# Performance work log

Measured on AMD Instinct MI355X. Metric: run time of the kernel, lower is better.

Reference implementation:

```python
import jax, jax.numpy as jnp
import numpy as np

L, B, T, D, H, M = 2, 4, 1024, 256, 4, 1024
EPS = 1e-5  # hk.LayerNorm default


def setup_inputs() -> dict:
    key = jax.random.key(0)
    ks = jax.random.split(key, 12)
    s_in = (2.0 / D) ** 0.5       # VarianceScaling(2.0), fan_in = D
    s_o = (2.0 / (H * D)) ** 0.5  # fan_in = H*D for final projection
    s_m = (1.0 / M) ** 0.5
    g = lambda k, shape, s: jax.random.normal(k, shape, jnp.float32) * s
    return {
        "queries": g(ks[0], (B, T, D), 1.0),
        "Wq": g(ks[1], (L, D, H * D), s_in),
        "bq": jnp.zeros((L, H * D), jnp.float32),
        "Wk": g(ks[2], (L, D, H * D), s_in),
        "bk": jnp.zeros((L, H * D), jnp.float32),
        "Wv": g(ks[3], (L, D, H * D), s_in),
        "bv": jnp.zeros((L, H * D), jnp.float32),
        "Wo": g(ks[4], (L, H * D, D), s_o),
        "bo": jnp.zeros((L, D), jnp.float32),
        "ln1_s": jnp.ones((L, D), jnp.float32),
        "ln1_b": jnp.zeros((L, D), jnp.float32),
        "W1": g(ks[5], (L, D, M), s_in),
        "b1": jnp.zeros((L, M), jnp.float32),
        "W2": g(ks[6], (L, M, D), s_m),
        "b2": jnp.zeros((L, D), jnp.float32),
        "ln2_s": jnp.ones((L, D), jnp.float32),
        "ln2_b": jnp.zeros((L, D), jnp.float32),
    }


def _layernorm(x, s, o):
    m = jnp.mean(x, axis=-1, keepdims=True)
    v = jnp.var(x, axis=-1, keepdims=True)
    return (x - m) * jax.lax.rsqrt(v + EPS) * s + o


def _block(x, Wq, bq, Wk, bk, Wv, bv, Wo, bo, ln1_s, ln1_b, W1, b1, W2, b2, ln2_s, ln2_b):
    # Multi-head self-attention with per-head dim = D (key_size == qkv_size)
    q = (x @ Wq + bq).reshape(B, T, H, D)
    k = (x @ Wk + bk).reshape(B, T, H, D)
    v = (x @ Wv + bv).reshape(B, T, H, D)
    q = q / jnp.sqrt(jnp.float32(D))
    attn = jnp.einsum('bqhd,bkhd->bhqk', q, k)   # [B,H,T,T]
    attn = jax.nn.softmax(attn, axis=-1)
    o = jnp.einsum('bhqk,bkhd->bqhd', attn, v).reshape(B, T, H * D)
    o = o @ Wo + bo
    # post-norm residual 1
    x = _layernorm(o + x, ln1_s, ln1_b)
    # MLP: Linear(D->M) + ReLU + Linear(M->D)
    h = jax.nn.relu(x @ W1 + b1)
    m = h @ W2 + b2
    return _layernorm(m + x, ln2_s, ln2_b)


def reference(queries, Wq, bq, Wk, bk, Wv, bv, Wo, bo, ln1_s, ln1_b,
              W1, b1, W2, b2, ln2_s, ln2_b):
    x = queries
    for i in range(L):
        x = _block(x, Wq[i], bq[i], Wk[i], bk[i], Wv[i], bv[i], Wo[i], bo[i],
                   ln1_s[i], ln1_b[i], W1[i], b1[i], W2[i], b2[i],
                   ln2_s[i], ln2_b[i])
    return x
```

## Files before the change

kernel.cpp:

```cpp
#include <hip/hip_runtime.h>
#include <hip/hip_bf16.h>

#define CL 2
#define CB 4
#define CT 1024
#define CD 256
#define CH 4
#define CM 1024
#define CHD (CH * CD)
#define NROW (CB * CT)

typedef unsigned short ushort_t;
typedef __attribute__((ext_vector_type(8))) short short8v;
typedef __attribute__((ext_vector_type(4))) float float4v;

#define LOG2E 1.44269504088896f

__device__ __forceinline__ float bf2f(unsigned short u) {
    return __uint_as_float(((unsigned int)u) << 16);
}
__device__ __forceinline__ unsigned short f2bf(float f) {
    unsigned int x = __float_as_uint(f);
    return (unsigned short)((x + 0x7fffu + ((x >> 16) & 1u)) >> 16);
}

__global__ __launch_bounds__(256) void detect_kernel(
    const ushort_t* __restrict__ w, int n, int* __restrict__ flag)
{
    __shared__ int red[256];
    int c = 0;
    for (int i = threadIdx.x; i < n; i += 256) {
        float v = bf2f(w[i]);
        if (!(fabsf(v) <= 1e6f)) c++;
    }
    red[threadIdx.x] = c;
    __syncthreads();
    for (int s = 128; s > 0; s >>= 1) {
        if (threadIdx.x < s) red[threadIdx.x] += red[threadIdx.x + s];
        __syncthreads();
    }
    if (threadIdx.x == 0) flag[0] = (red[0] < 8) ? 1 : 0;
}

__global__ __launch_bounds__(256) void tconv_all(
    const void* __restrict__ Wq, const void* __restrict__ Wk,
    const void* __restrict__ Wv, const void* __restrict__ W1,
    ushort_t* __restrict__ wqkvT, ushort_t* __restrict__ w1T,
    const int* __restrict__ flagp)
{
    const int fbf = *flagp;
    const int z = blockIdx.z;
    const int which = z >> 1, l = z & 1;
    const void* in = (which == 0) ? Wq : (which == 1) ? Wk
                   : (which == 2) ? Wv : W1;
    ushort_t* out = (which < 3)
        ? wqkvT + (long)l * 3072 * 256 + (long)which * 1024 * 256
        : w1T + (long)l * 1024 * 256;
    const long zi = (long)l * 262144;

    __shared__ float tile[32][33];
    const int r0 = blockIdx.y * 32;
    const int c0 = blockIdx.x * 32;
    const int tx = threadIdx.x & 31;
    const int ty = threadIdx.x >> 5;
#pragma unroll
    for (int i = 0; i < 32; i += 8) {
        const long idx = zi + (long)(r0 + ty + i) * 1024 + c0 + tx;
        tile[ty + i][tx] = fbf ? bf2f(((const ushort_t*)in)[idx])
                               : ((const float*)in)[idx];
    }
    __syncthreads();
#pragma unroll
    for (int i = 0; i < 32; i += 8)
        out[(long)(c0 + ty + i) * 256 + r0 + tx] = f2bf(tile[tx][ty + i]);
}

__global__ __launch_bounds__(256) void qkv_tconv(
    const ushort_t* __restrict__ A, const ushort_t* __restrict__ B,
    const void* __restrict__ bq, const void* __restrict__ bk,
    const void* __restrict__ bv, ushort_t* __restrict__ qk,
    ushort_t* __restrict__ vT,
    const void* __restrict__ Wo, const void* __restrict__ W2,
    ushort_t* __restrict__ wscr,
    long boff, long ioff, const int* __restrict__ flagp)
{
    __shared__ __align__(16) ushort_t As[128 * 40];
    __shared__ __align__(16) ushort_t Bs[128 * 40];
    __shared__ float tile[32][33];

    const int fbf = *flagp;
    const int bx = blockIdx.x;
    const int tid = threadIdx.x;

    if (bx >= 768) {
        const int t = bx - 768;
        const int zx = t & 7;
        const int zy = (t >> 3) & 31;
        const int zz = t >> 8;
        const void* in = zz ? W2 : Wo;
        ushort_t* out = wscr + (long)zz * 262144;
        const int r0 = zy * 32;
        const int c0 = zx * 32;
        const int tx = tid & 31;
        const int ty = tid >> 5;
#pragma unroll
        for (int i = 0; i < 32; i += 8) {
            const long idx = ioff + (long)(r0 + ty + i) * 256 + c0 + tx;
            tile[ty + i][tx] = fbf ? bf2f(((const ushort_t*)in)[idx])
                                   : ((const float*)in)[idx];
        }
        __syncthreads();
#pragma unroll
        for (int i = 0; i < 32; i += 8)
            out[(long)(c0 + ty + i) * 1024 + r0 + tx] = f2bf(tile[tx][ty + i]);
        return;
    }

    const int nt = bx % 24;
    const int mt = bx / 24;
    const long m0 = (long)mt * 128;
    const long n0 = (long)nt * 128;

    const int wave = tid >> 6;
    const int lane = tid & 63;
    const int quad = lane >> 4;
    const int lrow = lane & 15;
    const int wm = (wave >> 1) * 64;
    const int wn = (wave & 1) * 64;

    float4v acc[4][4];
#pragma unroll
    for (int i = 0; i < 4; ++i)
#pragma unroll
        for (int j = 0; j < 4; ++j)
            acc[i][j] = (float4v){0.f, 0.f, 0.f, 0.f};

    for (int k0 = 0; k0 < 256; k0 += 32) {
        __syncthreads();
#pragma unroll
        for (int p = 0; p < 2; ++p) {
            const int c = p * 256 + tid;
            const int row = c >> 2;
            const int kk = (c & 3) << 3;
            *reinterpret_cast<short8v*>(&As[row * 40 + kk]) =
                *reinterpret_cast<const short8v*>(&A[(m0 + row) * 256 + k0 + kk]);
            *reinterpret_cast<short8v*>(&Bs[row * 40 + kk]) =
                *reinterpret_cast<const short8v*>(&B[(n0 + row) * 256 + k0 + kk]);
        }
        __syncthreads();

        short8v af[4], bfv[4];
#pragma unroll
        for (int i = 0; i < 4; ++i) {
            af[i]  = *reinterpret_cast<const short8v*>(&As[(wm + i * 16 + lrow) * 40 + quad * 8]);
            bfv[i] = *reinterpret_cast<const short8v*>(&Bs[(wn + i * 16 + lrow) * 40 + quad * 8]);
        }
#pragma unroll
        for (int mi = 0; mi < 4; ++mi)
#pragma unroll
            for (int ni = 0; ni < 4; ++ni)
                acc[mi][ni] = __builtin_amdgcn_mfma_f32_16x16x32_bf16(
                    af[mi], bfv[ni], acc[mi][ni], 0, 0, 0);
    }

#pragma unroll
    for (int mi = 0; mi < 4; ++mi) {
#pragma unroll
        for (int ni = 0; ni < 4; ++ni) {
            const long col = n0 + wn + ni * 16 + lrow;
            const long row0 = m0 + wm + mi * 16 + quad * 4;
            const void* bp;
            long bn;
            if (col < 1024)      { bp = bq; bn = col; }
            else if (col < 2048) { bp = bk; bn = col - 1024; }
            else                 { bp = bv; bn = col - 2048; }
            const float bias = fbf ? bf2f(((const ushort_t*)bp)[boff + bn])
                                   : ((const float*)bp)[boff + bn];
            if (col < 2048) {
#pragma unroll
                for (int r = 0; r < 4; ++r)
                    qk[(row0 + r) * 2048 + col] = f2bf(acc[mi][ni][r] + bias);
            } else {
                const long d = col - 2048;
                const long addr = ((row0 >> 10) << 2) * 262144 + d * 1024 + (row0 & 1023);
                ushort4 u;
                u.x = f2bf(acc[mi][ni][0] + bias);
                u.y = f2bf(acc[mi][ni][1] + bias);
                u.z = f2bf(acc[mi][ni][2] + bias);
                u.w = f2bf(acc[mi][ni][3] + bias);
                *reinterpret_cast<ushort4*>(&vT[addr]) = u;
            }
        }
    }
}

template <int AMODE>
__global__ __launch_bounds__(256) void mgemm64s(
    const ushort_t* __restrict__ A, const ushort_t* __restrict__ Ap1,
    const float2* __restrict__ ml, const ushort_t* __restrict__ B,
    float* __restrict__ P, int K2, int lda, int ldb)
{
    const int z = blockIdx.z;
    const long m0 = (long)blockIdx.y * 64;
    const long n0 = (long)blockIdx.x * 64;
    const int k_beg = z * K2;

    __shared__ __align__(16) ushort_t As[64 * 72];
    __shared__ __align__(16) ushort_t Bs[64 * 72];

    const int tid = threadIdx.x;
    const int wave = tid >> 6;
    const int lane = tid & 63;
    const int quad = lane >> 4;
    const int lrow = lane & 15;
    const int wm = (wave >> 1) * 32;
    const int wn = (wave & 1) * 32;

    const int ar = tid >> 2;
    const int ak = (tid & 3) << 3;

    float s0h[2] = {0.f, 0.f}, s1h[2] = {0.f, 0.f};
    if constexpr (AMODE == 1) {
        const long m = m0 + ar;
        const int bhbase = ((int)(m >> 10) << 2);
        const int trow = (int)(m & 1023);
        const int h0 = k_beg >> 8;
#pragma unroll
        for (int i = 0; i < 2; ++i) {
            const int bh = bhbase + h0 + i;
            const float2 v0 = ml[bh * 1024 + trow];
            const float2 v1 = ml[(16 + bh) * 1024 + trow];
            const float mm = fmaxf(v0.x, v1.x);
            const float a0 = exp2f(v0.x - mm);
            const float a1 = exp2f(v1.x - mm);
            const float inv = 1.0f / (v0.y * a0 + v1.y * a1);
            s0h[i] = a0 * inv;
            s1h[i] = a1 * inv;
        }
    }

    float4v acc[2][2];
#pragma unroll
    for (int i = 0; i < 2; ++i)
#pragma unroll
        for (int j = 0; j < 2; ++j)
            acc[i][j] = (float4v){0.f, 0.f, 0.f, 0.f};

    for (int k0 = k_beg; k0 < k_beg + K2; k0 += 64) {
        __syncthreads();
#pragma unroll
        for (int p = 0; p < 2; ++p) {
            const int kc = p * 32 + ak;
            if constexpr (AMODE == 0) {
                *reinterpret_cast<short8v*>(&As[ar * 72 + kc]) =
                    *reinterpret_cast<const short8v*>(&A[(m0 + ar) * (long)lda + k0 + kc]);
            } else {
                const long m = m0 + ar;
                const int hi = ((k0 + kc) >> 8) - (k_beg >> 8);
                const float s0 = s0h[hi], s1 = s1h[hi];
                const ushort4 u0a = *reinterpret_cast<const ushort4*>(&A[m * 1024 + k0 + kc]);
                const ushort4 u0b = *reinterpret_cast<const ushort4*>(&A[m * 1024 + k0 + kc + 4]);
                const ushort4 u1a = *reinterpret_cast<const ushort4*>(&Ap1[m * 1024 + k0 + kc]);
                const ushort4 u1b = *reinterpret_cast<const ushort4*>(&Ap1[m * 1024 + k0 + kc + 4]);
                short8v t8;
                t8[0] = (short)f2bf(bf2f(u0a.x) * s0 + bf2f(u1a.x) * s1);
                t8[1] = (short)f2bf(bf2f(u0a.y) * s0 + bf2f(u1a.y) * s1);
                t8[2] = (short)f2bf(bf2f(u0a.z) * s0 + bf2f(u1a.z) * s1);
                t8[3] = (short)f2bf(bf2f(u0a.w) * s0 + bf2f(u1a.w) * s1);
                t8[4] = (short)f2bf(bf2f(u0b.x) * s0 + bf2f(u1b.x) * s1);
                t8[5] = (short)f2bf(bf2f(u0b.y) * s0 + bf2f(u1b.y) * s1);
                t8[6] = (short)f2bf(bf2f(u0b.z) * s0 + bf2f(u1b.z) * s1);
                t8[7] = (short)f2bf(bf2f(u0b.w) * s0 + bf2f(u1b.w) * s1);
                *reinterpret_cast<short8v*>(&As[ar * 72 + kc]) = t8;
            }
            *reinterpret_cast<short8v*>(&Bs[ar * 72 + kc]) =
                *reinterpret_cast<const short8v*>(&B[(n0 + ar) * (long)ldb + k0 + kc]);
        }
        __syncthreads();

#pragma unroll
        for (int kk = 0; kk < 2; ++kk) {
            short8v af[2], bfv[2];
#pragma unroll
            for (int i = 0; i < 2; ++i) {
                af[i]  = *reinterpret_cast<const short8v*>(
                    &As[(wm + i * 16 + lrow) * 72 + kk * 32 + quad * 8]);
                bfv[i] = *reinterpret_cast<const short8v*>(
                    &Bs[(wn + i * 16 + lrow) * 72 + kk * 32 + quad * 8]);
            }
#pragma unroll
            for (int mi = 0; mi < 2; ++mi)
#pragma unroll
                for (int ni = 0; ni < 2; ++ni)
                    acc[mi][ni] = __builtin_amdgcn_mfma_f32_16x16x32_bf16(
                        af[mi], bfv[ni], acc[mi][ni], 0, 0, 0);
        }
    }

    float* Pz = P + (long)z * NROW * CD;
#pragma unroll
    for (int mi = 0; mi < 2; ++mi)
#pragma unroll
        for (int ni = 0; ni < 2; ++ni) {
            const long col = n0 + wn + ni * 16 + lrow;
            const long row0 = m0 + wm + mi * 16 + quad * 4;
#pragma unroll
            for (int r = 0; r < 4; ++r)
                Pz[(row0 + r) * CD + col] = acc[mi][ni][r];
        }
}

template <int RELU>
__global__ __launch_bounds__(256) void mgemm64b(
    const ushort_t* __restrict__ A, const ushort_t* __restrict__ B,
    const void* __restrict__ bias, ushort_t* __restrict__ C,
    int K, int lda, int ldb, int ldc, long boff,
    const int* __restrict__ flagp)
{
    const long m0 = (long)blockIdx.y * 64;
    const long n0 = (long)blockIdx.x * 64;

    __shared__ __align__(16) ushort_t As[64 * 72];
    __shared__ __align__(16) ushort_t Bs[64 * 72];

    const int tid = threadIdx.x;
    const int wave = tid >> 6;
    const int lane = tid & 63;
    const int quad = lane >> 4;
    const int lrow = lane & 15;
    const int wm = (wave >> 1) * 32;
    const int wn = (wave & 1) * 32;

    const int ar = tid >> 2;
    const int ak = (tid & 3) << 3;

    float4v acc[2][2];
#pragma unroll
    for (int i = 0; i < 2; ++i)
#pragma unroll
        for (int j = 0; j < 2; ++j)
            acc[i][j] = (float4v){0.f, 0.f, 0.f, 0.f};

    for (int k0 = 0; k0 < K; k0 += 64) {
        __syncthreads();
#pragma unroll
        for (int p = 0; p < 2; ++p) {
            const int kc = p * 32 + ak;
            *reinterpret_cast<short8v*>(&As[ar * 72 + kc]) =
                *reinterpret_cast<const short8v*>(&A[(m0 + ar) * (long)lda + k0 + kc]);
            *reinterpret_cast<short8v*>(&Bs[ar * 72 + kc]) =
                *reinterpret_cast<const short8v*>(&B[(n0 + ar) * (long)ldb + k0 + kc]);
        }
        __syncthreads();

#pragma unroll
        for (int kk = 0; kk < 2; ++kk) {
            short8v af[2], bfv[2];
#pragma unroll
            for (int i = 0; i < 2; ++i) {
                af[i]  = *reinterpret_cast<const short8v*>(
                    &As[(wm + i * 16 + lrow) * 72 + kk * 32 + quad * 8]);
                bfv[i] = *reinterpret_cast<const short8v*>(
                    &Bs[(wn + i * 16 + lrow) * 72 + kk * 32 + quad * 8]);
            }
#pragma unroll
            for (int mi = 0; mi < 2; ++mi)
#pragma unroll
                for (int ni = 0; ni < 2; ++ni)
                    acc[mi][ni] = __builtin_amdgcn_mfma_f32_16x16x32_bf16(
                        af[mi], bfv[ni], acc[mi][ni], 0, 0, 0);
        }
    }

    const int fbf = *flagp;
#pragma unroll
    for (int mi = 0; mi < 2; ++mi)
#pragma unroll
        for (int ni = 0; ni < 2; ++ni) {
            const long col = n0 + wn + ni * 16 + lrow;
            const long row0 = m0 + wm + mi * 16 + quad * 4;
            const float bv = fbf ? bf2f(((const ushort_t*)bias)[boff + col])
                                 : ((const float*)bias)[boff + col];
#pragma unroll
            for (int r = 0; r < 4; ++r) {
                float v = acc[mi][ni][r] + bv;
                if (RELU) v = fmaxf(v, 0.f);
                C[(row0 + r) * (long)ldc + col] = f2bf(v);
            }
        }
}

__global__ __launch_bounds__(256) void flash_attn(
    const ushort_t* __restrict__ qk, const ushort_t* __restrict__ vT,
    ushort_t* __restrict__ op0, ushort_t* __restrict__ op1,
    float2* __restrict__ ml)
{
    const int bx = blockIdx.x;
    const int bh = bx & 15;
    const int qt = (bx >> 4) & 15;
    const int ck = bx >> 8;
    const int b = bh >> 2, h = bh & 3;

    __shared__ __align__(16) ushort_t Ks[32 * 264];
    __shared__ __align__(16) ushort_t Vs[256 * 40];
    __shared__ __align__(16) ushort_t Ps[4][16 * 40];

    const int tid = threadIdx.x;
    const int wave = tid >> 6;
    const int lane = tid & 63;
    const int quad = lane >> 4;
    const int lrow = lane & 15;

    const long qrow0 = (long)b * CT + qt * 64;
    const int qcol = h * 256;
    const int kcol = 1024 + h * 256;
    const long vbase = (long)bh * 256 * 1024;
    const float SC = 0.0625f * LOG2E;

    short8v qf[8];
#pragma unroll
    for (int kk = 0; kk < 8; ++kk)
        qf[kk] = *reinterpret_cast<const short8v*>(
            &qk[(qrow0 + wave * 16 + lrow) * 2048 + qcol + kk * 32 + quad * 8]);

    float mrun = -1e30f, lrun = 0.f;
    float4v oacc[16];
#pragma unroll
    for (int i = 0; i < 16; ++i) oacc[i] = (float4v){0.f, 0.f, 0.f, 0.f};

    const int t_beg = ck * 512;
    for (int t0 = t_beg; t0 < t_beg + 512; t0 += 32) {
        __syncthreads();
#pragma unroll
        for (int p = 0; p < 4; ++p) {
            const int c = p * 256 + tid;
            {
                const int r = c >> 5, col = (c & 31) * 8;
                *reinterpret_cast<short8v*>(&Ks[r * 264 + col]) =
                    *reinterpret_cast<const short8v*>(
                        &qk[((long)b * CT + t0 + r) * 2048 + kcol + col]);
            }
            {
                const int r = c >> 2, col = (c & 3) * 8;
                *reinterpret_cast<short8v*>(&Vs[r * 40 + col]) =
                    *reinterpret_cast<const short8v*>(
                        &vT[vbase + (long)r * 1024 + t0 + col]);
            }
        }
        __syncthreads();

        float4v sacc[2];
        sacc[0] = (float4v){0.f, 0.f, 0.f, 0.f};
        sacc[1] = (float4v){0.f, 0.f, 0.f, 0.f};
#pragma unroll
        for (int kk = 0; kk < 8; ++kk) {
#pragma unroll
            for (int ni = 0; ni < 2; ++ni) {
                short8v bk = *reinterpret_cast<const short8v*>(
                    &Ks[(ni * 16 + lrow) * 264 + kk * 32 + quad * 8]);
                sacc[ni] = __builtin_amdgcn_mfma_f32_16x16x32_bf16(
                    bk, qf[kk], sacc[ni], 0, 0, 0);
            }
        }
#pragma unroll
        for (int ni = 0; ni < 2; ++ni)
#pragma unroll
            for (int r = 0; r < 4; ++r)
                sacc[ni][r] *= SC;

        float mx = fmaxf(fmaxf(fmaxf(sacc[0][0], sacc[0][1]),
                               fmaxf(sacc[0][2], sacc[0][3])),
                         fmaxf(fmaxf(sacc[1][0], sacc[1][1]),
                               fmaxf(sacc[1][2], sacc[1][3])));
        mx = fmaxf(mx, __shfl_xor(mx, 16));
        mx = fmaxf(mx, __shfl_xor(mx, 32));

        if (__ballot(mx > mrun + 1.0f) != 0ull) {
            const float mnew = fmaxf(mrun, mx);
            const float alpha = exp2f(mrun - mnew);
            mrun = mnew;
            lrun *= alpha;
            float a4[4];
#pragma unroll
            for (int r = 0; r < 4; ++r)
                a4[r] = __shfl(alpha, quad * 4 + r);
#pragma unroll
            for (int ni = 0; ni < 16; ++ni)
#pragma unroll
                for (int r = 0; r < 4; ++r)
                    oacc[ni][r] *= a4[r];
        }

        float s = 0.f;
#pragma unroll
        for (int ni = 0; ni < 2; ++ni) {
            ushort4 pu;
#pragma unroll
            for (int r = 0; r < 4; ++r) {
                const float pv = exp2f(sacc[ni][r] - mrun);
                s += pv;
                (&pu.x)[r] = f2bf(pv);
            }
            *reinterpret_cast<ushort4*>(
                &Ps[wave][lrow * 40 + ni * 16 + quad * 4]) = pu;
        }
        s += __shfl_xor(s, 16);
        s += __shfl_xor(s, 32);
        lrun += s;

        {
            short8v ap = *reinterpret_cast<const short8v*>(
                &Ps[wave][lrow * 40 + quad * 8]);
#pragma unroll
            for (int ni = 0; ni < 16; ++ni) {
                short8v bv = *reinterpret_cast<const short8v*>(
                    &Vs[(ni * 16 + lrow) * 40 + quad * 8]);
                oacc[ni] = __builtin_amdgcn_mfma_f32_16x16x32_bf16(
                    ap, bv, oacc[ni], 0, 0, 0);
            }
        }
    }

    if (quad == 0)
        ml[((ck << 4) + bh) * 1024 + qt * 64 + wave * 16 + lrow] =
            make_float2(mrun, lrun);

    ushort_t* op = ck ? op1 : op0;
#pragma unroll
    for (int ni = 0; ni < 16; ++ni)
#pragma unroll
        for (int r = 0; r < 4; ++r)
            op[(qrow0 + wave * 16 + quad * 4 + r) * 1024 + (h << 8) + ni * 16 + lrow]
                = f2bf(oacc[ni][r]);
}

template <int FINAL>
__global__ __launch_bounds__(256) void ln_p(
    const float* __restrict__ p, const void* __restrict__ gb, long gboff,
    const ushort_t* __restrict__ res, const void* __restrict__ sc,
    const void* __restrict__ bi, void* __restrict__ out, long loff,
    const int* __restrict__ flagp)
{
    const int fbf = *flagp;
    const long row = (long)blockIdx.x * CD;
    const int t = threadIdx.x;
    const float gbv = fbf ? bf2f(((const ushort_t*)gb)[gboff + t])
                          : ((const float*)gb)[gboff + t];
    const float x = p[row + t] + p[(long)NROW * CD + row + t] + gbv + bf2f(res[row + t]);

    __shared__ float r1[256];
    __shared__ float r2[256];
    r1[t] = x;
    r2[t] = x * x;
    __syncthreads();
    for (int s = 128; s > 0; s >>= 1) {
        if (t < s) { r1[t] += r1[t + s]; r2[t] += r2[t + s]; }
        __syncthreads();
    }
    const float mean = r1[0] * (1.0f / CD);
    const float var = r2[0] * (1.0f / CD) - mean * mean;
    const float rstd = rsqrtf(var + 1e-5f);
    const float s_v = fbf ? bf2f(((const ushort_t*)sc)[loff + t]) : ((const float*)sc)[loff + t];
    const float b_v = fbf ? bf2f(((const ushort_t*)bi)[loff + t]) : ((const float*)bi)[loff + t];
    const float y = (x - mean) * rstd * s_v + b_v;
    if constexpr (FINAL) {
        if (fbf) ((ushort_t*)out)[row + t] = f2bf(y);
        else     ((float*)out)[row + t] = y;
    } else {
        ((ushort_t*)out)[row + t] = f2bf(y);
    }
}

__global__ __launch_bounds__(256) void in_convert(
    const void* __restrict__ in, ushort_t* __restrict__ x,
    const int* __restrict__ flagp)
{
    const int fbf = *flagp;
    const long i = ((long)blockIdx.x * 256 + threadIdx.x) << 2;
    if (fbf) {
        *reinterpret_cast<ushort4*>(x + i) =
            *reinterpret_cast<const ushort4*>((const ushort_t*)in + i);
    } else {
        float4 f = *reinterpret_cast<const float4*>((const float*)in + i);
        ushort4 u;
        u.x = f2bf(f.x); u.y = f2bf(f.y); u.z = f2bf(f.z); u.w = f2bf(f.w);
        *reinterpret_cast<ushort4*>(x + i) = u;
    }
}

extern "C" void kernel_launch(void* const* d_in, const int* in_sizes, int n_in,
                              void* d_out, int out_size, void* d_ws, size_t ws_size,
                              hipStream_t stream)
{
    const void* queries = d_in[0];
    const void* Wq = d_in[1];  const void* bq = d_in[2];
    const void* Wk = d_in[3];  const void* bk = d_in[4];
    const void* Wv = d_in[5];  const void* bv = d_in[6];
    const void* Wo = d_in[7];  const void* bo = d_in[8];
    const void* ln1s = d_in[9];  const void* ln1b = d_in[10];
    const void* W1 = d_in[11]; const void* b1 = d_in[12];
    const void* W2 = d_in[13]; const void* b2 = d_in[14];
    const void* ln2s = d_in[15]; const void* ln2b = d_in[16];

    char* p = (char*)d_ws;
    int* flagp = (int*)p;             p += 256;
    ushort_t* wqkvT = (ushort_t*)p;   p += (long)CL * 3072 * 256 * 2;
    ushort_t* w1T   = (ushort_t*)p;   p += (long)CL * 1024 * 256 * 2;
    ushort_t* wscr  = (ushort_t*)p;   p += (long)2 * 256 * 1024 * 2;
    ushort_t* xa    = (ushort_t*)p;   p += (long)NROW * CD * 2;
    ushort_t* qk    = (ushort_t*)p;   p += (long)NROW * 2048 * 2;
    ushort_t* vT    = (ushort_t*)p;   p += (long)16 * 256 * 1024 * 2;
    ushort_t* op0   = (ushort_t*)p;   p += (long)NROW * 1024 * 2;
    ushort_t* op1   = (ushort_t*)p;   p += (long)NROW * 1024 * 2;
    float2*   ml    = (float2*)p;     p += (long)2 * 16 * 1024 * 8;
    ushort_t* h     = vT;
    float*    pgem  = (float*)qk;

    detect_kernel<<<1, 256, 0, stream>>>((const ushort_t*)Wq, 2048, flagp);
    tconv_all<<<dim3(32, 8, 8), 256, 0, stream>>>(
        Wq, Wk, Wv, W1, wqkvT, w1T, flagp);
    in_convert<<<(NROW * CD) / 1024, 256, 0, stream>>>(queries, xa, flagp);

    for (int l = 0; l < CL; ++l) {
        qkv_tconv<<<dim3(1280, 1, 1), 256, 0, stream>>>(
            xa, wqkvT + (long)l * 3072 * 256, bq, bk, bv, qk, vT,
            Wo, W2, wscr, (long)l * 1024, (long)l * 1024 * 256, flagp);
        flash_attn<<<512, 256, 0, stream>>>(qk, vT, op0, op1, ml);
        mgemm64s<1><<<dim3(4, 64, 2), 256, 0, stream>>>(
            op0, op1, ml, wscr, pgem, 512, 1024, 1024);
        ln_p<0><<<NROW, 256, 0, stream>>>(pgem, bo, (long)l * 256, xa,
                                          ln1s, ln1b, xa, (long)l * 256, flagp);
        mgemm64b<1><<<dim3(16, 64, 1), 256, 0, stream>>>(
            xa, w1T + (long)l * 1024 * 256, b1, h,
            256, 256, 256, 1024, (long)l * 1024, flagp);
        mgemm64s<0><<<dim3(4, 64, 2), 256, 0, stream>>>(
            h, nullptr, nullptr, wscr + 262144, pgem, 512, 1024, 1024);
        if (l == CL - 1)
            ln_p<1><<<NROW, 256, 0, stream>>>(pgem, b2, (long)l * 256, xa,
                                              ln2s, ln2b, d_out, (long)l * 256, flagp);
        else
            ln_p<0><<<NROW, 256, 0, stream>>>(pgem, b2, (long)l * 256, xa,
                                              ln2s, ln2b, xa, (long)l * 256, flagp);
    }
}
```

Measured before the change: 305.2 us.

## Merge prepass kernels, widen GEMM K tiles, and use wave-per-row layernorm

Fuses the weight transpose and input conversion into a single prepass launch. Doubles the K step of the QKV GEMM to 64 so it needs half as many barrier rounds. Replaces the 64x64 MLP up-projection tile with a 128x64 tile, four waves each covering 32 rows, for more reuse of each loaded B tile. Rewrites layernorm so each wave handles one row using vectorized float4 loads and shuffle reductions instead of a shared-memory tree. The larger tiles use more LDS and registers, which may lower occupancy.

Result: slower. 312.9 us (+2.5%).

```diff
diff --git a/kernel.cpp b/kernel.cpp
--- a/kernel.cpp
+++ b/kernel.cpp
@@ -42,14 +42,32 @@
     if (threadIdx.x == 0) flag[0] = (red[0] < 8) ? 1 : 0;
 }
 
-__global__ __launch_bounds__(256) void tconv_all(
+__global__ __launch_bounds__(256) void prepass_kernel(
     const void* __restrict__ Wq, const void* __restrict__ Wk,
     const void* __restrict__ Wv, const void* __restrict__ W1,
     ushort_t* __restrict__ wqkvT, ushort_t* __restrict__ w1T,
+    const void* __restrict__ queries, ushort_t* __restrict__ xa,
     const int* __restrict__ flagp)
 {
     const int fbf = *flagp;
-    const int z = blockIdx.z;
+    const int bx = blockIdx.x;
+    const int tid = threadIdx.x;
+
+    if (bx >= 2048) {
+        const long i = ((long)(bx - 2048) * 256 + tid) << 2;
+        if (fbf) {
+            *reinterpret_cast<ushort4*>(xa + i) =
+                *reinterpret_cast<const ushort4*>((const ushort_t*)queries + i);
+        } else {
+            float4 f = *reinterpret_cast<const float4*>((const float*)queries + i);
+            ushort4 u;
+            u.x = f2bf(f.x); u.y = f2bf(f.y); u.z = f2bf(f.z); u.w = f2bf(f.w);
+            *reinterpret_cast<ushort4*>(xa + i) = u;
+        }
+        return;
+    }
+
+    const int z = bx >> 8;
     const int which = z >> 1, l = z & 1;
     const void* in = (which == 0) ? Wq : (which == 1) ? Wk
                    : (which == 2) ? Wv : W1;
@@ -59,10 +77,10 @@
     const long zi = (long)l * 262144;
 
     __shared__ float tile[32][33];
-    const int r0 = blockIdx.y * 32;
-    const int c0 = blockIdx.x * 32;
-    const int tx = threadIdx.x & 31;
-    const int ty = threadIdx.x >> 5;
+    const int r0 = ((bx >> 5) & 7) * 32;
+    const int c0 = (bx & 31) * 32;
+    const int tx = tid & 31;
+    const int ty = tid >> 5;
 #pragma unroll
     for (int i = 0; i < 32; i += 8) {
         const long idx = zi + (long)(r0 + ty + i) * 1024 + c0 + tx;
@@ -84,8 +102,8 @@
     ushort_t* __restrict__ wscr,
     long boff, long ioff, const int* __restrict__ flagp)
 {
-    __shared__ __align__(16) ushort_t As[128 * 40];
-    __shared__ __align__(16) ushort_t Bs[128 * 40];
+    __shared__ __align__(16) ushort_t As[128 * 72];
+    __shared__ __align__(16) ushort_t Bs[128 * 72];
     __shared__ float tile[32][33];
 
     const int fbf = *flagp;
@@ -135,32 +153,37 @@
         for (int j = 0; j < 4; ++j)
             acc[i][j] = (float4v){0.f, 0.f, 0.f, 0.f};
 
-    for (int k0 = 0; k0 < 256; k0 += 32) {
-        __syncthreads();
-#pragma unroll
-        for (int p = 0; p < 2; ++p) {
+    for (int k0 = 0; k0 < 256; k0 += 64) {
+        __syncthreads();
+#pragma unroll
+        for (int p = 0; p < 4; ++p) {
             const int c = p * 256 + tid;
-            const int row = c >> 2;
-            const int kk = (c & 3) << 3;
-            *reinterpret_cast<short8v*>(&As[row * 40 + kk]) =
-                *reinterpret_cast<const short8v*>(&A[(m0 + row) * 256 + k0 + kk]);
-            *reinterpret_cast<short8v*>(&Bs[row * 40 + kk]) =
-                *reinterpret_cast<const short8v*>(&B[(n0 + row) * 256 + k0 + kk]);
-        }
-        __syncthreads();
-
-        short8v af[4], bfv[4];
-#pragma unroll
-        for (int i = 0; i < 4; ++i) {
-            af[i]  = *reinterpret_cast<const short8v*>(&As[(wm + i * 16 + lrow) * 40 + quad * 8]);
-            bfv[i] = *reinterpret_cast<const short8v*>(&Bs[(wn + i * 16 + lrow) * 40 + quad * 8]);
-        }
-#pragma unroll
-        for (int mi = 0; mi < 4; ++mi)
-#pragma unroll
-            for (int ni = 0; ni < 4; ++ni)
-                acc[mi][ni] = __builtin_amdgcn_mfma_f32_16x16x32_bf16(
-                    af[mi], bfv[ni], acc[mi][ni], 0, 0, 0);
+            const int row = c >> 3;
+            const int kc = (c & 7) << 3;
+            *reinterpret_cast<short8v*>(&As[row * 72 + kc]) =
+                *reinterpret_cast<const short8v*>(&A[(m0 + row) * 256 + k0 + kc]);
+            *reinterpret_cast<short8v*>(&Bs[row * 72 + kc]) =
+                *reinterpret_cast<const short8v*>(&B[(n0 + row) * 256 + k0 + kc]);
+        }
+        __syncthreads();
+
+#pragma unroll
+        for (int kk = 0; kk < 2; ++kk) {
+            short8v af[4], bfv[4];
+#pragma unroll
+            for (int i = 0; i < 4; ++i) {
+                af[i]  = *reinterpret_cast<const short8v*>(
+                    &As[(wm + i * 16 + lrow) * 72 + kk * 32 + quad * 8]);
+                bfv[i] = *reinterpret_cast<const short8v*>(
+                    &Bs[(wn + i * 16 + lrow) * 72 + kk * 32 + quad * 8]);
+            }
+#pragma unroll
+            for (int mi = 0; mi < 4; ++mi)
+#pragma unroll
+                for (int ni = 0; ni < 4; ++ni)
+                    acc[mi][ni] = __builtin_amdgcn_mfma_f32_16x16x32_bf16(
+                        af[mi], bfv[ni], acc[mi][ni], 0, 0, 0);
+        }
     }
 
 #pragma unroll
@@ -311,16 +334,16 @@
 }
 
 template <int RELU>
-__global__ __launch_bounds__(256) void mgemm64b(
+__global__ __launch_bounds__(256) void mgemm128b(
     const ushort_t* __restrict__ A, const ushort_t* __restrict__ B,
     const void* __restrict__ bias, ushort_t* __restrict__ C,
     int K, int lda, int ldb, int ldc, long boff,
     const int* __restrict__ flagp)
 {
-    const long m0 = (long)blockIdx.y * 64;
+    const long m0 = (long)blockIdx.y * 128;
     const long n0 = (long)blockIdx.x * 64;
 
-    __shared__ __align__(16) ushort_t As[64 * 72];
+    __shared__ __align__(16) ushort_t As[128 * 72];
     __shared__ __align__(16) ushort_t Bs[64 * 72];
 
     const int tid = threadIdx.x;
@@ -328,45 +351,50 @@
     const int lane = tid & 63;
     const int quad = lane >> 4;
     const int lrow = lane & 15;
-    const int wm = (wave >> 1) * 32;
-    const int wn = (wave & 1) * 32;
-
-    const int ar = tid >> 2;
-    const int ak = (tid & 3) << 3;
-
-    float4v acc[2][2];
+    const int wm = wave * 32;
+
+    float4v acc[2][4];
 #pragma unroll
     for (int i = 0; i < 2; ++i)
 #pragma unroll
-        for (int j = 0; j < 2; ++j)
+        for (int j = 0; j < 4; ++j)
             acc[i][j] = (float4v){0.f, 0.f, 0.f, 0.f};
 
     for (int k0 = 0; k0 < K; k0 += 64) {
         __syncthreads();
 #pragma unroll
+        for (int p = 0; p < 4; ++p) {
+            const int c = p * 256 + tid;
+            const int row = c >> 3;
+            const int kc = (c & 7) << 3;
+            *reinterpret_cast<short8v*>(&As[row * 72 + kc]) =
+                *reinterpret_cast<const short8v*>(&A[(m0 + row) * (long)lda + k0 + kc]);
+        }
+#pragma unroll
         for (int p = 0; p < 2; ++p) {
-            const int kc = p * 32 + ak;
-            *reinterpret_cast<short8v*>(&As[ar * 72 + kc]) =
-                *reinterpret_cast<const short8v*>(&A[(m0 + ar) * (long)lda + k0 + kc]);
-            *reinterpret_cast<short8v*>(&Bs[ar * 72 + kc]) =
-                *reinterpret_cast<const short8v*>(&B[(n0 + ar) * (long)ldb + k0 + kc]);
+            const int c = p * 256 + tid;
+            const int row = c >> 3;
+            const int kc = (c & 7) << 3;
+            *reinterpret_cast<short8v*>(&Bs[row * 72 + kc]) =
+                *reinterpret_cast<const short8v*>(&B[(n0 + row) * (long)ldb + k0 + kc]);
         }
         __syncthreads();
 
 #pragma unroll
         for (int kk = 0; kk < 2; ++kk) {
-            short8v af[2], bfv[2];
-#pragma unroll
-            for (int i = 0; i < 2; ++i) {
-                af[i]  = *reinterpret_cast<const short8v*>(
+            short8v af[2], bfv[4];
+#pragma unroll
+            for (int i = 0; i < 2; ++i)
+                af[i] = *reinterpret_cast<const short8v*>(
                     &As[(wm + i * 16 + lrow) * 72 + kk * 32 + quad * 8]);
+#pragma unroll
+            for (int i = 0; i < 4; ++i)
                 bfv[i] = *reinterpret_cast<const short8v*>(
-                    &Bs[(wn + i * 16 + lrow) * 72 + kk * 32 + quad * 8]);
-            }
+                    &Bs[(i * 16 + lrow) * 72 + kk * 32 + quad * 8]);
 #pragma unroll
             for (int mi = 0; mi < 2; ++mi)
 #pragma unroll
-                for (int ni = 0; ni < 2; ++ni)
+                for (int ni = 0; ni < 4; ++ni)
                     acc[mi][ni] = __builtin_amdgcn_mfma_f32_16x16x32_bf16(
                         af[mi], bfv[ni], acc[mi][ni], 0, 0, 0);
         }
@@ -376,8 +404,8 @@
 #pragma unroll
     for (int mi = 0; mi < 2; ++mi)
 #pragma unroll
-        for (int ni = 0; ni < 2; ++ni) {
-            const long col = n0 + wn + ni * 16 + lrow;
+        for (int ni = 0; ni < 4; ++ni) {
+            const long col = n0 + ni * 16 + lrow;
             const long row0 = m0 + wm + mi * 16 + quad * 4;
             const float bv = fbf ? bf2f(((const ushort_t*)bias)[boff + col])
                                  : ((const float*)bias)[boff + col];
@@ -542,49 +570,68 @@
     const int* __restrict__ flagp)
 {
     const int fbf = *flagp;
-    const long row = (long)blockIdx.x * CD;
-    const int t = threadIdx.x;
-    const float gbv = fbf ? bf2f(((const ushort_t*)gb)[gboff + t])
-                          : ((const float*)gb)[gboff + t];
-    const float x = p[row + t] + p[(long)NROW * CD + row + t] + gbv + bf2f(res[row + t]);
-
-    __shared__ float r1[256];
-    __shared__ float r2[256];
-    r1[t] = x;
-    r2[t] = x * x;
-    __syncthreads();
-    for (int s = 128; s > 0; s >>= 1) {
-        if (t < s) { r1[t] += r1[t + s]; r2[t] += r2[t + s]; }
-        __syncthreads();
-    }
-    const float mean = r1[0] * (1.0f / CD);
-    const float var = r2[0] * (1.0f / CD) - mean * mean;
+    const int wave = threadIdx.x >> 6;
+    const int lane = threadIdx.x & 63;
+    const long base = ((long)blockIdx.x * 4 + wave) * CD;
+    const int c0 = lane << 2;
+
+    const float4 p0 = *reinterpret_cast<const float4*>(&p[base + c0]);
+    const float4 p1 = *reinterpret_cast<const float4*>(&p[(long)NROW * CD + base + c0]);
+    const ushort4 rs = *reinterpret_cast<const ushort4*>(&res[base + c0]);
+    float g[4];
+    if (fbf) {
+        const ushort4 gu = *reinterpret_cast<const ushort4*>(
+            &((const ushort_t*)gb)[gboff + c0]);
+        g[0] = bf2f(gu.x); g[1] = bf2f(gu.y); g[2] = bf2f(gu.z); g[3] = bf2f(gu.w);
+    } else {
+        const float4 gf = *reinterpret_cast<const float4*>(
+            &((const float*)gb)[gboff + c0]);
+        g[0] = gf.x; g[1] = gf.y; g[2] = gf.z; g[3] = gf.w;
+    }
+    float x[4];
+    x[0] = p0.x + p1.x + g[0] + bf2f(rs.x);
+    x[1] = p0.y + p1.y + g[1] + bf2f(rs.y);
+    x[2] = p0.z + p1.z + g[2] + bf2f(rs.z);
+    x[3] = p0.w + p1.w + g[3] + bf2f(rs.w);
+
+    float s1 = (x[0] + x[1]) + (x[2] + x[3]);
+    float s2 = (x[0] * x[0] + x[1] * x[1]) + (x[2] * x[2] + x[3] * x[3]);
+#pragma unroll
+    for (int sh = 1; sh < 64; sh <<= 1) {
+        s1 += __shfl_xor(s1, sh);
+        s2 += __shfl_xor(s2, sh);
+    }
+    const float mean = s1 * (1.0f / CD);
+    const float var = s2 * (1.0f / CD) - mean * mean;
     const float rstd = rsqrtf(var + 1e-5f);
-    const float s_v = fbf ? bf2f(((const ushort_t*)sc)[loff + t]) : ((const float*)sc)[loff + t];
-    const float b_v = fbf ? bf2f(((const ushort_t*)bi)[loff + t]) : ((const float*)bi)[loff + t];
-    const float y = (x - mean) * rstd * s_v + b_v;
-    if constexpr (FINAL) {
-        if (fbf) ((ushort_t*)out)[row + t] = f2bf(y);
-        else     ((float*)out)[row + t] = y;
+
+    float scv[4], biv[4];
+    if (fbf) {
+        const ushort4 su = *reinterpret_cast<const ushort4*>(
+            &((const ushort_t*)sc)[loff + c0]);
+        const ushort4 bu = *reinterpret_cast<const ushort4*>(
+            &((const ushort_t*)bi)[loff + c0]);
+        scv[0] = bf2f(su.x); scv[1] = bf2f(su.y); scv[2] = bf2f(su.z); scv[3] = bf2f(su.w);
+        biv[0] = bf2f(bu.x); biv[1] = bf2f(bu.y); biv[2] = bf2f(bu.z); biv[3] = bf2f(bu.w);
     } else {
-        ((ushort_t*)out)[row + t] = f2bf(y);
-    }
-}
-
-__global__ __launch_bounds__(256) void in_convert(
-    const void* __restrict__ in, ushort_t* __restrict__ x,
-    const int* __restrict__ flagp)
-{
-    const int fbf = *flagp;
-    const long i = ((long)blockIdx.x * 256 + threadIdx.x) << 2;
-    if (fbf) {
-        *reinterpret_cast<ushort4*>(x + i) =
-            *reinterpret_cast<const ushort4*>((const ushort_t*)in + i);
+        const float4 sf = *reinterpret_cast<const float4*>(&((const float*)sc)[loff + c0]);
+        const float4 bf = *reinterpret_cast<const float4*>(&((const float*)bi)[loff + c0]);
+        scv[0] = sf.x; scv[1] = sf.y; scv[2] = sf.z; scv[3] = sf.w;
+        biv[0] = bf.x; biv[1] = bf.y; biv[2] = bf.z; biv[3] = bf.w;
+    }
+    float y[4];
+#pragma unroll
+    for (int j = 0; j < 4; ++j)
+        y[j] = (x[j] - mean) * rstd * scv[j] + biv[j];
+
+    if (FINAL && !fbf) {
+        float4 f;
+        f.x = y[0]; f.y = y[1]; f.z = y[2]; f.w = y[3];
+        *reinterpret_cast<float4*>(&((float*)out)[base + c0]) = f;
     } else {
-        float4 f = *reinterpret_cast<const float4*>((const float*)in + i);
         ushort4 u;
-        u.x = f2bf(f.x); u.y = f2bf(f.y); u.z = f2bf(f.z); u.w = f2bf(f.w);
-        *reinterpret_cast<ushort4*>(x + i) = u;
+        u.x = f2bf(y[0]); u.y = f2bf(y[1]); u.z = f2bf(y[2]); u.w = f2bf(y[3]);
+        *reinterpret_cast<ushort4*>(&((ushort_t*)out)[base + c0]) = u;
     }
 }
 
@@ -617,9 +664,8 @@
     float*    pgem  = (float*)qk;
 
     detect_kernel<<<1, 256, 0, stream>>>((const ushort_t*)Wq, 2048, flagp);
-    tconv_all<<<dim3(32, 8, 8), 256, 0, stream>>>(
-        Wq, Wk, Wv, W1, wqkvT, w1T, flagp);
-    in_convert<<<(NROW * CD) / 1024, 256, 0, stream>>>(queries, xa, flagp);
+    prepass_kernel<<<3072, 256, 0, stream>>>(
+        Wq, Wk, Wv, W1, wqkvT, w1T, queries, xa, flagp);
 
     for (int l = 0; l < CL; ++l) {
         qkv_tconv<<<dim3(1280, 1, 1), 256, 0, stream>>>(
@@ -628,18 +674,18 @@
         flash_attn<<<512, 256, 0, stream>>>(qk, vT, op0, op1, ml);
         mgemm64s<1><<<dim3(4, 64, 2), 256, 0, stream>>>(
             op0, op1, ml, wscr, pgem, 512, 1024, 1024);
-        ln_p<0><<<NROW, 256, 0, stream>>>(pgem, bo, (long)l * 256, xa,
-                                          ln1s, ln1b, xa, (long)l * 256, flagp);
-        mgemm64b<1><<<dim3(16, 64, 1), 256, 0, stream>>>(
+        ln_p<0><<<NROW / 4, 256, 0, stream>>>(pgem, bo, (long)l * 256, xa,
+                                              ln1s, ln1b, xa, (long)l * 256, flagp);
+        mgemm128b<1><<<dim3(16, 32, 1), 256, 0, stream>>>(
             xa, w1T + (long)l * 1024 * 256, b1, h,
             256, 256, 256, 1024, (long)l * 1024, flagp);
         mgemm64s<0><<<dim3(4, 64, 2), 256, 0, stream>>>(
             h, nullptr, nullptr, wscr + 262144, pgem, 512, 1024, 1024);
         if (l == CL - 1)
-            ln_p<1><<<NROW, 256, 0, stream>>>(pgem, b2, (long)l * 256, xa,
-                                              ln2s, ln2b, d_out, (long)l * 256, flagp);
+            ln_p<1><<<NROW / 4, 256, 0, stream>>>(pgem, b2, (long)l * 256, xa,
+                                                  ln2s, ln2b, d_out, (long)l * 256, flagp);
         else
-            ln_p<0><<<NROW, 256, 0, stream>>>(pgem, b2, (long)l * 256, xa,
-                                              ln2s, ln2b, xa, (long)l * 256, flagp);
-    }
-}
+            ln_p<0><<<NROW / 4, 256, 0, stream>>>(pgem, b2, (long)l * 256, xa,
+                                                  ln2s, ln2b, xa, (long)l * 256, flagp);
+    }
+}
```
